# Kernel optimization log

Measured on AMD Instinct MI355X. Metric: run time of the kernel, lower is better.

The kernel has to match this reference:

```python
import jax, jax.numpy as jnp
import numpy as np

N_EDGES = 10_000_000
N_RELS = 64
N_POL = 3


def setup_inputs() -> dict:
    key = jax.random.key(0)
    k0, k1, k2, k3, k4 = jax.random.split(key, 5)
    prnt_probs = jax.random.uniform(k0, (N_EDGES, N_POL), dtype=jnp.float32)
    child_probs = jax.random.uniform(k1, (N_EDGES, N_POL), dtype=jnp.float32)
    rels = jax.random.randint(k2, (N_EDGES,), 0, N_RELS, dtype=jnp.int64 if jax.config.jax_enable_x64 else jnp.int32)
    # learned parameters (torch inits them to ones/constants; random keeps grads nontrivial)
    M = jax.random.normal(k3, (N_RELS, N_POL, N_POL), dtype=jnp.float32)
    beta = jax.random.uniform(k4, (N_RELS, N_POL), dtype=jnp.float32)
    z_epsilon = jnp.float32(0.01)
    scale_factor = jnp.float32(21.0)
    return {
        "var_sfx": 0,
        "prnt_probs": prnt_probs,
        "child_probs": child_probs,
        "rels": rels,
        "M": M,
        "beta": beta,
        "z_epsilon": z_epsilon,
        "scale_factor": scale_factor,
    }


def _scale(prnt_probs, child_probs, z_epsilon, scale_factor):
    # entropy of the clipped, renormalized blend of parent+child distributions
    z = jnp.maximum(z_epsilon, prnt_probs + child_probs)  # [E,3]
    z = z / jnp.sum(z, axis=-1, keepdims=True)
    entropy = -jnp.sum(z * jnp.log(z), axis=-1)  # [E]
    # cosine similarity between parent and child distributions
    cos = jnp.sum(prnt_probs * child_probs, axis=-1)
    norm = jnp.linalg.norm(prnt_probs, axis=-1) * jnp.linalg.norm(child_probs, axis=-1)
    norm = jnp.where(norm == 0, jnp.ones_like(norm), norm)
    cos = 1.1 + cos / norm
    return scale_factor * cos / entropy  # [E]


def reference(var_sfx, prnt_probs, child_probs, rels, M, beta, z_epsilon, scale_factor):
    # relation-indexed gather + tiny 3x3 matvec + softmax
    # (inputs guarantee all row sums > 0, so the torch nonzero masks select every row)
    scores = jnp.einsum('nij,nj->ni', M[rels], child_probs)  # [E,3]
    child = jax.nn.softmax(scores, axis=-1)
    b = beta[rels]  # [E,3]
    alpha = (1.0 - b) * prnt_probs + b * child
    scale = _scale(prnt_probs, child, z_epsilon, scale_factor)
    return alpha * scale[:, None]
```

## Files before the change

### kernel.cpp

```cpp
#include <hip/hip_runtime.h>

#define TPB 256
#define N_RELS 64
#define EPT 4

typedef float f4 __attribute__((ext_vector_type(4)));
typedef int   i4 __attribute__((ext_vector_type(4)));

__device__ __forceinline__ void edge_compute(
    const float* __restrict__ sMB, int r,
    float p0, float p1, float p2,
    float c0, float c1, float c2,
    float zeps, float sf, float* __restrict__ o)
{
    const f4* mb = (const f4*)(sMB + r * 12);
    f4 q0 = mb[0], q1 = mb[1], q2 = mb[2];

    float s0 = q0.x * c0 + q0.y * c1 + q0.z * c2;
    float s1 = q0.w * c0 + q1.x * c1 + q1.y * c2;
    float s2 = q1.z * c0 + q1.w * c1 + q2.x * c2;

    float mx = fmaxf(fmaxf(s0, s1), s2);
    float e0 = __expf(s0 - mx);
    float e1 = __expf(s1 - mx);
    float e2 = __expf(s2 - mx);
    float inv = __fdividef(1.0f, e0 + e1 + e2);
    float ch0 = e0 * inv, ch1 = e1 * inv, ch2 = e2 * inv;

    float a0 = p0 + q2.y * (ch0 - p0);
    float a1 = p1 + q2.z * (ch1 - p1);
    float a2 = p2 + q2.w * (ch2 - p2);

    float z0 = fmaxf(zeps, p0 + ch0);
    float z1 = fmaxf(zeps, p1 + ch1);
    float z2 = fmaxf(zeps, p2 + ch2);
    float zinv = __fdividef(1.0f, z0 + z1 + z2);
    float zn0 = z0 * zinv, zn1 = z1 * zinv, zn2 = z2 * zinv;
    float ent = -(zn0 * __logf(zn0) + zn1 * __logf(zn1) + zn2 * __logf(zn2));

    float dot = p0 * ch0 + p1 * ch1 + p2 * ch2;
    float np2 = p0 * p0 + p1 * p1 + p2 * p2;
    float nc2 = ch0 * ch0 + ch1 * ch1 + ch2 * ch2;
    float prod = np2 * nc2;
    float cosn = (prod > 0.0f) ? dot * rsqrtf(prod) : dot;
    float cosv = 1.1f + cosn;

    float scale = sf * cosv * __fdividef(1.0f, ent);

    o[0] = a0 * scale;
    o[1] = a1 * scale;
    o[2] = a2 * scale;
}

__global__ __launch_bounds__(TPB, 8) void alpha_kernel(
    const float* __restrict__ prnt,
    const float* __restrict__ child,
    const int*   __restrict__ rels,
    const float* __restrict__ M,
    const float* __restrict__ beta,
    const float* __restrict__ zeps_p,
    const float* __restrict__ sf_p,
    float* __restrict__ out,
    int n_groups,
    long n_edges)
{
    __shared__ float sMB[N_RELS * 12];
    for (int i = threadIdx.x; i < N_RELS * 12; i += TPB) {
        int r = i / 12, j = i - r * 12;
        sMB[i] = (j < 9) ? M[r * 9 + j] : beta[r * 3 + (j - 9)];
    }
    __syncthreads();

    const float zeps = *zeps_p;
    const float sf   = *sf_p;

    const int nthreads = gridDim.x * TPB;
    const int tid0 = blockIdx.x * TPB + threadIdx.x;

    for (int g = tid0; g < n_groups; g += nthreads) {
        const i4* r4 = (const i4*)rels  + g;
        const f4* p4 = (const f4*)prnt  + (size_t)g * 3;
        const f4* c4 = (const f4*)child + (size_t)g * 3;

        i4 R = *r4;
        f4 P4[3], C4[3];
        #pragma unroll
        for (int i = 0; i < 3; ++i) P4[i] = p4[i];
        #pragma unroll
        for (int i = 0; i < 3; ++i) C4[i] = c4[i];

        int Rr[EPT] = {R.x, R.y, R.z, R.w};
        const float* P = (const float*)P4;
        const float* C = (const float*)C4;

        float O[EPT * 3];
        #pragma unroll
        for (int e = 0; e < EPT; ++e) {
            edge_compute(sMB, Rr[e],
                         P[3 * e], P[3 * e + 1], P[3 * e + 2],
                         C[3 * e], C[3 * e + 1], C[3 * e + 2],
                         zeps, sf, &O[3 * e]);
        }

        f4* o4 = (f4*)out + (size_t)g * 3;
        const f4* Ov = (const f4*)O;
        #pragma unroll
        for (int i = 0; i < 3; ++i) o4[i] = Ov[i];
    }

    long tail_start = (long)n_groups * EPT;
    long t = (long)tid0;
    long eidx = tail_start + t;
    if (eidx < n_edges) {
        float o[3];
        edge_compute(sMB, rels[eidx],
                     prnt[eidx * 3 + 0], prnt[eidx * 3 + 1], prnt[eidx * 3 + 2],
                     child[eidx * 3 + 0], child[eidx * 3 + 1], child[eidx * 3 + 2],
                     zeps, sf, o);
        out[eidx * 3 + 0] = o[0];
        out[eidx * 3 + 1] = o[1];
        out[eidx * 3 + 2] = o[2];
    }
}

extern "C" void kernel_launch(void* const* d_in, const int* in_sizes, int n_in,
                              void* d_out, int out_size, void* d_ws, size_t ws_size,
                              hipStream_t stream) {
    const float* prnt  = (const float*)d_in[1];
    const float* child = (const float*)d_in[2];
    const int*   rels  = (const int*)d_in[3];
    const float* M     = (const float*)d_in[4];
    const float* beta  = (const float*)d_in[5];
    const float* zeps  = (const float*)d_in[6];
    const float* sf    = (const float*)d_in[7];
    float* out = (float*)d_out;

    long n_edges  = in_sizes[3];
    int  n_groups = (int)(n_edges / EPT);

    int blocks = 2048;
    long need = ((long)n_groups + TPB - 1) / TPB;
    if (need < blocks) blocks = (int)(need > 0 ? need : 1);

    alpha_kernel<<<blocks, TPB, 0, stream>>>(prnt, child, rels, M, beta,
                                             zeps, sf, out, n_groups, n_edges);
}
```

Measured before the change: 334.3 us.

## Double-buffer group loads in registers and use raw exp2/log2 intrinsics

Restructures the grid-stride loop to prefetch the next group of edges into registers while computing the current one, aiming to hide global memory latency. Also folds log2(e) into M and the scale factor so softmax and entropy can use hardware exp2/log2/rcp/rsq intrinsics, and drops the softmax max-subtraction. This raises register pressure (launch bound occupancy hint removed) and risks exp overflow for large scores.

Measured after the change: 375.2 us. +12.2%, slower.

```diff
diff --git a/kernel.cpp b/kernel.cpp
--- a/kernel.cpp
+++ b/kernel.cpp
@@ -3,28 +3,37 @@
 #define TPB 256
 #define N_RELS 64
 #define EPT 4
+#define LOG2E 1.4426950408889634f
 
 typedef float f4 __attribute__((ext_vector_type(4)));
 typedef int   i4 __attribute__((ext_vector_type(4)));
 
-__device__ __forceinline__ void edge_compute(
-    const float* __restrict__ sMB, int r,
-    float p0, float p1, float p2,
-    float c0, float c1, float c2,
-    float zeps, float sf, float* __restrict__ o)
+struct G { i4 R; f4 P0, P1, P2, C0, C1, C2; };
+
+__device__ __forceinline__ void load_group(G& g, const int* __restrict__ rels,
+                                           const float* __restrict__ prnt,
+                                           const float* __restrict__ child, int idx) {
+    g.R  = ((const i4*)rels)[idx];
+    const f4* p = (const f4*)prnt  + (size_t)idx * 3;
+    const f4* c = (const f4*)child + (size_t)idx * 3;
+    g.P0 = p[0]; g.P1 = p[1]; g.P2 = p[2];
+    g.C0 = c[0]; g.C1 = c[1]; g.C2 = c[2];
+}
+
+__device__ __forceinline__ void edge_compute(const f4* __restrict__ sMB4, int r,
+    float p0, float p1, float p2, float c0, float c1, float c2,
+    float zeps, float sf2, float* __restrict__ o)
 {
-    const f4* mb = (const f4*)(sMB + r * 12);
+    const f4* mb = sMB4 + r * 3;
     f4 q0 = mb[0], q1 = mb[1], q2 = mb[2];
 
     float s0 = q0.x * c0 + q0.y * c1 + q0.z * c2;
     float s1 = q0.w * c0 + q1.x * c1 + q1.y * c2;
     float s2 = q1.z * c0 + q1.w * c1 + q2.x * c2;
-
-    float mx = fmaxf(fmaxf(s0, s1), s2);
-    float e0 = __expf(s0 - mx);
-    float e1 = __expf(s1 - mx);
-    float e2 = __expf(s2 - mx);
-    float inv = __fdividef(1.0f, e0 + e1 + e2);
+    float e0 = __builtin_amdgcn_exp2f(s0);
+    float e1 = __builtin_amdgcn_exp2f(s1);
+    float e2 = __builtin_amdgcn_exp2f(s2);
+    float inv = __builtin_amdgcn_rcpf(e0 + e1 + e2);
     float ch0 = e0 * inv, ch1 = e1 * inv, ch2 = e2 * inv;
 
     float a0 = p0 + q2.y * (ch0 - p0);
@@ -34,25 +43,44 @@
     float z0 = fmaxf(zeps, p0 + ch0);
     float z1 = fmaxf(zeps, p1 + ch1);
     float z2 = fmaxf(zeps, p2 + ch2);
-    float zinv = __fdividef(1.0f, z0 + z1 + z2);
+    float zinv = __builtin_amdgcn_rcpf(z0 + z1 + z2);
     float zn0 = z0 * zinv, zn1 = z1 * zinv, zn2 = z2 * zinv;
-    float ent = -(zn0 * __logf(zn0) + zn1 * __logf(zn1) + zn2 * __logf(zn2));
+    float ent2 = -(zn0 * __builtin_amdgcn_logf(zn0)
+                 + zn1 * __builtin_amdgcn_logf(zn1)
+                 + zn2 * __builtin_amdgcn_logf(zn2));
 
     float dot = p0 * ch0 + p1 * ch1 + p2 * ch2;
     float np2 = p0 * p0 + p1 * p1 + p2 * p2;
     float nc2 = ch0 * ch0 + ch1 * ch1 + ch2 * ch2;
     float prod = np2 * nc2;
-    float cosn = (prod > 0.0f) ? dot * rsqrtf(prod) : dot;
-    float cosv = 1.1f + cosn;
+    float cosn = (prod > 0.0f) ? dot * __builtin_amdgcn_rsqf(prod) : dot;
 
-    float scale = sf * cosv * __fdividef(1.0f, ent);
+    float scale = sf2 * (1.1f + cosn) * __builtin_amdgcn_rcpf(ent2);
 
     o[0] = a0 * scale;
     o[1] = a1 * scale;
     o[2] = a2 * scale;
 }
 
-__global__ __launch_bounds__(TPB, 8) void alpha_kernel(
+__device__ __forceinline__ void compute_store(const G& g, const f4* __restrict__ sMB4,
+    float zeps, float sf2, float* __restrict__ out, int idx)
+{
+    int   R[EPT] = {g.R.x, g.R.y, g.R.z, g.R.w};
+    float P[12]  = {g.P0.x, g.P0.y, g.P0.z, g.P0.w, g.P1.x, g.P1.y, g.P1.z, g.P1.w,
+                    g.P2.x, g.P2.y, g.P2.z, g.P2.w};
+    float C[12]  = {g.C0.x, g.C0.y, g.C0.z, g.C0.w, g.C1.x, g.C1.y, g.C1.z, g.C1.w,
+                    g.C2.x, g.C2.y, g.C2.z, g.C2.w};
+    float O[12];
+    #pragma unroll
+    for (int e = 0; e < EPT; ++e)
+        edge_compute(sMB4, R[e], P[3*e], P[3*e+1], P[3*e+2],
+                     C[3*e], C[3*e+1], C[3*e+2], zeps, sf2, &O[3*e]);
+    f4* o4 = (f4*)out + (size_t)idx * 3;
+    const f4* Ov = (const f4*)O;
+    o4[0] = Ov[0]; o4[1] = Ov[1]; o4[2] = Ov[2];
+}
+
+__global__ __launch_bounds__(TPB) void alpha_kernel(
     const float* __restrict__ prnt,
     const float* __restrict__ child,
     const int*   __restrict__ rels,
@@ -64,59 +92,47 @@
     int n_groups,
     long n_edges)
 {
-    __shared__ float sMB[N_RELS * 12];
-    for (int i = threadIdx.x; i < N_RELS * 12; i += TPB) {
-        int r = i / 12, j = i - r * 12;
-        sMB[i] = (j < 9) ? M[r * 9 + j] : beta[r * 3 + (j - 9)];
+    __shared__ f4 sMB4[N_RELS * 3];
+    {
+        float* sMB = (float*)sMB4;
+        for (int i = threadIdx.x; i < N_RELS * 12; i += TPB) {
+            int r = i / 12, j = i - r * 12;
+            sMB[i] = (j < 9) ? M[r * 9 + j] * LOG2E : beta[r * 3 + (j - 9)];
+        }
     }
     __syncthreads();
 
     const float zeps = *zeps_p;
-    const float sf   = *sf_p;
+    const float sf2  = *sf_p * LOG2E;
 
     const int nthreads = gridDim.x * TPB;
     const int tid0 = blockIdx.x * TPB + threadIdx.x;
 
-    for (int g = tid0; g < n_groups; g += nthreads) {
-        const i4* r4 = (const i4*)rels  + g;
-        const f4* p4 = (const f4*)prnt  + (size_t)g * 3;
-        const f4* c4 = (const f4*)child + (size_t)g * 3;
-
-        i4 R = *r4;
-        f4 P4[3], C4[3];
-        #pragma unroll
-        for (int i = 0; i < 3; ++i) P4[i] = p4[i];
-        #pragma unroll
-        for (int i = 0; i < 3; ++i) C4[i] = c4[i];
-
-        int Rr[EPT] = {R.x, R.y, R.z, R.w};
-        const float* P = (const float*)P4;
-        const float* C = (const float*)C4;
-
-        float O[EPT * 3];
-        #pragma unroll
-        for (int e = 0; e < EPT; ++e) {
-            edge_compute(sMB, Rr[e],
-                         P[3 * e], P[3 * e + 1], P[3 * e + 2],
-                         C[3 * e], C[3 * e + 1], C[3 * e + 2],
-                         zeps, sf, &O[3 * e]);
+    int g = tid0;
+    if (g < n_groups) {
+        G A, B;
+        load_group(A, rels, prnt, child, g);
+        while (true) {
+            int gn = g + nthreads;
+            if (gn < n_groups) load_group(B, rels, prnt, child, gn);
+            compute_store(A, sMB4, zeps, sf2, out, g);
+            if (gn >= n_groups) break;
+            g = gn;
+            gn = g + nthreads;
+            if (gn < n_groups) load_group(A, rels, prnt, child, gn);
+            compute_store(B, sMB4, zeps, sf2, out, g);
+            if (gn >= n_groups) break;
+            g = gn;
         }
-
-        f4* o4 = (f4*)out + (size_t)g * 3;
-        const f4* Ov = (const f4*)O;
-        #pragma unroll
-        for (int i = 0; i < 3; ++i) o4[i] = Ov[i];
     }
 
-    long tail_start = (long)n_groups * EPT;
-    long t = (long)tid0;
-    long eidx = tail_start + t;
+    long eidx = (long)n_groups * EPT + (long)tid0;
     if (eidx < n_edges) {
         float o[3];
-        edge_compute(sMB, rels[eidx],
+        edge_compute(sMB4, rels[eidx],
                      prnt[eidx * 3 + 0], prnt[eidx * 3 + 1], prnt[eidx * 3 + 2],
                      child[eidx * 3 + 0], child[eidx * 3 + 1], child[eidx * 3 + 2],
-                     zeps, sf, o);
+                     zeps, sf2, o);
         out[eidx * 3 + 0] = o[0];
         out[eidx * 3 + 1] = o[1];
         out[eidx * 3 + 2] = o[2];
```
